# Performance work log

Hardware: AMD Instinct MI355X
Metric: run time of the kernel (lower is better)

## Reference

```python
import jax, jax.numpy as jnp
import numpy as np

K = 3  # kernel size per spatial dim (stride=1, same padding)
MED_IDX = (K * K * K - 1) // 2  # torch.median returns the lower median; 27 taps -> index 13


def setup_inputs() -> dict:
    key = jax.random.key(0)
    x = jax.random.normal(key, (2, 1, 160, 160, 160), dtype=jnp.float32)
    return {"x": x}


def _median_pool3d(x):
    # same padding for k=3, stride=1: pad 1 (reflect) on each side of D, H, W
    xp = jnp.pad(x, ((0, 0), (0, 0), (1, 1), (1, 1), (1, 1)), mode="reflect")
    B, C, D, H, W = x.shape
    # gather the 27 shifted views (static slices; loop over fixed small kernel is fine)
    windows = [
        xp[:, :, i:i + D, j:j + H, l:l + W]
        for i in range(K) for j in range(K) for l in range(K)
    ]
    stack = jnp.stack(windows, axis=0)  # [27, B, C, D, H, W]
    # torch .median(dim=-1)[0] over 27 taps == sorted value at index 13
    return jnp.sort(stack, axis=0)[MED_IDX]


def reference(x):
    return _median_pool3d(x)
```

## Files before the change

kernel.cpp:

```cpp
#include <hip/hip_runtime.h>


typedef __fp16 hf2 __attribute__((ext_vector_type(2)));

#define DEV __device__ __forceinline__

DEV hf2 hmin2(hf2 a, hf2 b) { return __builtin_elementwise_min(a, b); }
DEV hf2 hmax2(hf2 a, hf2 b) { return __builtin_elementwise_max(a, b); }
DEV void ce(hf2& a, hf2& b) { hf2 lo = hmin2(a, b); hf2 hi = hmax2(a, b); a = lo; b = hi; }
DEV hf2 pk2(float a, float b) { return __builtin_amdgcn_cvt_pkrtz(a, b); }

DEV void sort3(hf2& a, hf2& b, hf2& c) { ce(a, b); ce(a, c); ce(b, c); }

DEV void merge21(hf2 a0, hf2 a1, hf2 b0, hf2 z[3]) {
    hf2 e0 = a0, e1 = b0; ce(e0, e1);
    z[0] = e0; z[1] = a1; z[2] = e1; ce(z[1], z[2]);
}
DEV void merge22(hf2 a0, hf2 a1, hf2 b0, hf2 b1, hf2 z[4]) {
    hf2 p0 = a0, p1 = b0; ce(p0, p1);
    hf2 q0 = a1, q1 = b1; ce(q0, q1);
    z[0] = p0; z[1] = q0; z[2] = p1; ce(z[1], z[2]); z[3] = q1;
}
DEV void merge31(hf2 a0, hf2 a1, hf2 a2, hf2 b0, hf2 z[4]) {
    hf2 e[3]; merge21(a0, a2, b0, e);
    z[0] = e[0]; z[1] = a1; z[2] = e[1]; ce(z[1], z[2]); z[3] = e[2];
}
DEV void merge32(hf2 a0, hf2 a1, hf2 a2, hf2 b0, hf2 b1, hf2 z[5]) {
    hf2 e[3]; merge21(a0, a2, b0, e);
    hf2 o0 = a1, o1 = b1; ce(o0, o1);
    z[0] = e[0];
    z[1] = o0; z[2] = e[1]; ce(z[1], z[2]);
    z[3] = o1; z[4] = e[2]; ce(z[3], z[4]);
}
DEV void merge33(const hf2 a[3], const hf2 b[3], hf2 z[6]) {
    hf2 e[4]; merge22(a[0], a[2], b[0], b[2], e);
    hf2 o0 = a[1], o1 = b[1]; ce(o0, o1);
    z[0] = e[0];
    z[1] = o0; z[2] = e[1]; ce(z[1], z[2]);
    z[3] = o1; z[4] = e[2]; ce(z[3], z[4]);
    z[5] = e[3];
}
DEV void merge63(const hf2 a[6], const hf2 b[3], hf2 z[9]) {
    hf2 e[5]; merge32(a[0], a[2], a[4], b[0], b[2], e);
    hf2 o[4]; merge31(a[1], a[3], a[5], b[1], o);
    z[0] = e[0];
    z[1] = o[0]; z[2] = e[1]; ce(z[1], z[2]);
    z[3] = o[1]; z[4] = e[2]; ce(z[3], z[4]);
    z[5] = o[2]; z[6] = e[3]; ce(z[5], z[6]);
    z[7] = o[3]; z[8] = e[4]; ce(z[7], z[8]);
}
DEV void merge44(const hf2 a[4], const hf2 b[4], hf2 z[8]) {
    hf2 e[4]; merge22(a[0], a[2], b[0], b[2], e);
    hf2 o[4]; merge22(a[1], a[3], b[1], b[3], o);
    z[0] = e[0];
    z[1] = o[0]; z[2] = e[1]; ce(z[1], z[2]);
    z[3] = o[1]; z[4] = e[2]; ce(z[3], z[4]);
    z[5] = o[2]; z[6] = e[3]; ce(z[5], z[6]);
    z[7] = o[3];
}
DEV void merge55(const hf2 a[5], const hf2 b[5], hf2 z[10]) {
    hf2 ae[3] = {a[0], a[2], a[4]}, be[3] = {b[0], b[2], b[4]};
    hf2 e[6]; merge33(ae, be, e);
    hf2 o[4]; merge22(a[1], a[3], b[1], b[3], o);
    z[0] = e[0];
    z[1] = o[0]; z[2] = e[1]; ce(z[1], z[2]);
    z[3] = o[1]; z[4] = e[2]; ce(z[3], z[4]);
    z[5] = o[2]; z[6] = e[3]; ce(z[5], z[6]);
    z[7] = o[3]; z[8] = e[4]; ce(z[7], z[8]);
    z[9] = e[5];
}
DEV void merge99(const hf2 a[9], const hf2 b[9], hf2 z[18]) {
    hf2 ae[5] = {a[0], a[2], a[4], a[6], a[8]};
    hf2 be[5] = {b[0], b[2], b[4], b[6], b[8]};
    hf2 e[10]; merge55(ae, be, e);
    hf2 ao[4] = {a[1], a[3], a[5], a[7]};
    hf2 bo[4] = {b[1], b[3], b[5], b[7]};
    hf2 o[8]; merge44(ao, bo, o);
    z[0] = e[0];
#pragma unroll
    for (int i = 0; i < 8; i++) {
        z[2 * i + 1] = o[i];
        z[2 * i + 2] = e[i + 1];
        ce(z[2 * i + 1], z[2 * i + 2]);
    }
    z[17] = e[9];
}

DEV void compute_m(const float* __restrict__ pb, const int ro[3], int c0, int x0, int c3,
                   hf2 M[9]) {
    hf2 r[3][3];
#pragma unroll
    for (int i = 0; i < 3; i++) {
        const float* p = pb + ro[i];
        float a = p[c0];
        float2 bc = *reinterpret_cast<const float2*>(p + x0);
        float d = p[c3];
        r[i][0] = pk2(a, bc.x);
        r[i][1] = pk2(bc.x, bc.y);
        r[i][2] = pk2(bc.y, d);
    }
    sort3(r[0][0], r[0][1], r[0][2]);
    sort3(r[1][0], r[1][1], r[1][2]);
    sort3(r[2][0], r[2][1], r[2][2]);
    hf2 s6[6]; merge33(r[0], r[1], s6);
    merge63(s6, r[2], M);
}

DEV hf2 sel13(const hf2 E[18], const hf2 R[9]) {
    hf2 m = E[13];
#pragma unroll
    for (int i = 0; i < 9; i++) m = hmin2(m, hmax2(R[i], E[12 - i]));
    return m;
}

constexpr int Bb = 2, Dd = 160, Hh = 160, Ww = 160;
constexpr int HW = Hh * Ww;
constexpr int WP = Ww / 2;
constexpr int TP = Hh * WP;
constexpr int CH = 10;
constexpr int NCH = Dd / CH;
constexpr int TOTAL = Bb * NCH * TP;

__global__ __launch_bounds__(256) void MedianPool3d_68994354642979_kernel(
    const float* __restrict__ in, float* __restrict__ out) {
    int tid = blockIdx.x * 256 + threadIdx.x;
    if (tid >= TOTAL) return;
    int t = tid % TP;
    int co = tid / TP;
    int b = co >> 4;
    int chunk = co & 15;
    int y = t / WP;
    int px = t - y * WP;
    int x0 = px * 2;

    int ym = (y == 0) ? 1 : y - 1;
    int yp = (y == Hh - 1) ? Hh - 2 : y + 1;
    int ro[3] = {ym * Ww, y * Ww, yp * Ww};
    int c0 = (x0 == 0) ? 1 : x0 - 1;
    int c3 = (x0 == Ww - 2) ? (Ww - 2) : x0 + 2;

    const float* base = in + (size_t)b * Dd * HW;
    float* ob = out + (size_t)b * Dd * HW;
    int z0 = chunk * CH;

    auto planeptr = [&](int p) {
        if (p < 0) p = -p;
        if (p >= Dd) p = 2 * Dd - 2 - p;
        return base + (size_t)p * HW;
    };

    hf2 SS[4][9];
    compute_m(planeptr(z0 - 1), ro, c0, x0, c3, SS[0]);
    compute_m(planeptr(z0),     ro, c0, x0, c3, SS[1]);
    compute_m(planeptr(z0 + 1), ro, c0, x0, c3, SS[2]);

#pragma unroll
    for (int j = 0; j < CH / 2; j++) {
        int z = z0 + 2 * j;
        int sm1 = (2 * j) & 3;
        int s0  = (2 * j + 1) & 3;
        int s1  = (2 * j + 2) & 3;
        int s2  = (2 * j + 3) & 3;

        compute_m(planeptr(z + 2), ro, c0, x0, c3, SS[s2]);

        hf2 E[18];
        merge99(SS[s0], SS[s1], E);
        hf2 med0 = sel13(E, SS[sm1]);
        hf2 med1 = sel13(E, SS[s2]);

        float* o0 = ob + (size_t)z * HW + ro[1] + x0;
        float* o1 = o0 + HW;
        *reinterpret_cast<float2*>(o0) = make_float2((float)med0[0], (float)med0[1]);
        *reinterpret_cast<float2*>(o1) = make_float2((float)med1[0], (float)med1[1]);

        if (j < CH / 2 - 1)
            compute_m(planeptr(z + 3), ro, c0, x0, c3, SS[sm1]);
    }
}

extern "C" void kernel_launch(void* const* d_in, const int* in_sizes, int n_in,
                              void* d_out, int out_size, void* d_ws, size_t ws_size,
                              hipStream_t stream) {
    const float* x = (const float*)d_in[0];
    float* out = (float*)d_out;
    constexpr int threads = 256;
    constexpr int blocks = TOTAL / threads;
    MedianPool3d_68994354642979_kernel<<<blocks, threads, 0, stream>>>(x, out);
}
```

Before: 31.51 us.

## Split plane load from sort and prefetch raw planes one iteration ahead

Plane loading is split out from the per-plane sorting network so raw float data for the next two depth planes can be loaded into double-buffered registers one loop iteration before use. The goal is to hide global-load latency behind the merge and select arithmetic. A five-slot sorted-plane ring replaces the four-slot one, and launch bounds now request 4 blocks per CU. The extra live registers for prefetched planes may raise pressure and cause spills under the tighter occupancy bound.

```diff
diff --git a/kernel.cpp b/kernel.cpp
--- a/kernel.cpp
+++ b/kernel.cpp
@@ -86,22 +86,28 @@
     z[17] = e[9];
 }
 
-DEV void compute_m(const float* __restrict__ pb, const int ro[3], int c0, int x0, int c3,
-                   hf2 M[9]) {
-    hf2 r[3][3];
+DEV void load_plane(const float* __restrict__ pb, const int ro[3], int c0, int x0, int c3,
+                    float R[12]) {
 #pragma unroll
     for (int i = 0; i < 3; i++) {
         const float* p = pb + ro[i];
-        float a = p[c0];
+        R[i * 4 + 0] = p[c0];
         float2 bc = *reinterpret_cast<const float2*>(p + x0);
-        float d = p[c3];
-        r[i][0] = pk2(a, bc.x);
-        r[i][1] = pk2(bc.x, bc.y);
-        r[i][2] = pk2(bc.y, d);
-    }
-    sort3(r[0][0], r[0][1], r[0][2]);
-    sort3(r[1][0], r[1][1], r[1][2]);
-    sort3(r[2][0], r[2][1], r[2][2]);
+        R[i * 4 + 1] = bc.x;
+        R[i * 4 + 2] = bc.y;
+        R[i * 4 + 3] = p[c3];
+    }
+}
+
+DEV void sort_plane(const float R[12], hf2 M[9]) {
+    hf2 r[3][3];
+#pragma unroll
+    for (int i = 0; i < 3; i++) {
+        r[i][0] = pk2(R[i * 4 + 0], R[i * 4 + 1]);
+        r[i][1] = pk2(R[i * 4 + 1], R[i * 4 + 2]);
+        r[i][2] = pk2(R[i * 4 + 2], R[i * 4 + 3]);
+        sort3(r[i][0], r[i][1], r[i][2]);
+    }
     hf2 s6[6]; merge33(r[0], r[1], s6);
     merge63(s6, r[2], M);
 }
@@ -121,7 +127,7 @@
 constexpr int NCH = Dd / CH;
 constexpr int TOTAL = Bb * NCH * TP;
 
-__global__ __launch_bounds__(256) void MedianPool3d_68994354642979_kernel(
+__global__ __launch_bounds__(256, 4) void MedianPool3d_68994354642979_kernel(
     const float* __restrict__ in, float* __restrict__ out) {
     int tid = blockIdx.x * 256 + threadIdx.x;
     if (tid >= TOTAL) return;
@@ -149,33 +155,49 @@
         return base + (size_t)p * HW;
     };
 
-    hf2 SS[4][9];
-    compute_m(planeptr(z0 - 1), ro, c0, x0, c3, SS[0]);
-    compute_m(planeptr(z0),     ro, c0, x0, c3, SS[1]);
-    compute_m(planeptr(z0 + 1), ro, c0, x0, c3, SS[2]);
+    hf2 SS[5][9];
+    float RT[2][2][12];
+
+    {
+        float P0[12], P1[12], P2[12];
+        load_plane(planeptr(z0 - 1), ro, c0, x0, c3, P0);
+        load_plane(planeptr(z0),     ro, c0, x0, c3, P1);
+        load_plane(planeptr(z0 + 1), ro, c0, x0, c3, P2);
+        sort_plane(P0, SS[0]);
+        sort_plane(P1, SS[1]);
+        sort_plane(P2, SS[2]);
+    }
+    load_plane(planeptr(z0 + 2), ro, c0, x0, c3, RT[0][0]);
+    load_plane(planeptr(z0 + 3), ro, c0, x0, c3, RT[0][1]);
 
 #pragma unroll
     for (int j = 0; j < CH / 2; j++) {
-        int z = z0 + 2 * j;
-        int sm1 = (2 * j) & 3;
-        int s0  = (2 * j + 1) & 3;
-        int s1  = (2 * j + 2) & 3;
-        int s2  = (2 * j + 3) & 3;
-
-        compute_m(planeptr(z + 2), ro, c0, x0, c3, SS[s2]);
+        const int z = z0 + 2 * j;
+        const int sA = (2 * j) % 5;
+        const int sB = (2 * j + 1) % 5;
+        const int sC = (2 * j + 2) % 5;
+        const int sD = (2 * j + 3) % 5;
+        const int sE = (2 * j + 4) % 5;
+        const int cb = j & 1, nb = cb ^ 1;
+
+        if (j + 1 < CH / 2) {
+            load_plane(planeptr(z + 4), ro, c0, x0, c3, RT[nb][0]);
+            if (2 * (j + 1) + 3 <= CH)
+                load_plane(planeptr(z + 5), ro, c0, x0, c3, RT[nb][1]);
+        }
+
+        sort_plane(RT[cb][0], SS[sD]);
+        if (2 * j + 3 <= CH) sort_plane(RT[cb][1], SS[sE]);
 
         hf2 E[18];
-        merge99(SS[s0], SS[s1], E);
-        hf2 med0 = sel13(E, SS[sm1]);
-        hf2 med1 = sel13(E, SS[s2]);
+        merge99(SS[sB], SS[sC], E);
+        hf2 med0 = sel13(E, SS[sA]);
+        hf2 med1 = sel13(E, SS[sD]);
 
         float* o0 = ob + (size_t)z * HW + ro[1] + x0;
         float* o1 = o0 + HW;
         *reinterpret_cast<float2*>(o0) = make_float2((float)med0[0], (float)med0[1]);
         *reinterpret_cast<float2*>(o1) = make_float2((float)med1[0], (float)med1[1]);
-
-        if (j < CH / 2 - 1)
-            compute_m(planeptr(z + 3), ro, c0, x0, c3, SS[sm1]);
     }
 }
 
```

Measured after the change: 31.58 us. About the same (+0.2%).

## Process four columns per thread with hf4 sorting networks and float4 I/O

Applied to the files above, without the earlier changes.

Each thread now covers four x positions instead of two. Taps are packed into 4-wide half vectors, so each min/max operates on two packed pairs, and loads and stores use float4. The depth chunk shrinks from 10 to 8, the launch-bounds occupancy hint is raised to 4, and the thread index is decomposed differently. Doubling the work per thread doubles register state and halves the thread count, which risks spills or lower occupancy.

```diff
diff --git a/kernel.cpp b/kernel.cpp
--- a/kernel.cpp
+++ b/kernel.cpp
@@ -2,66 +2,68 @@
 
 
 typedef __fp16 hf2 __attribute__((ext_vector_type(2)));
+typedef __fp16 hf4 __attribute__((ext_vector_type(4)));
 
 #define DEV __device__ __forceinline__
 
-DEV hf2 hmin2(hf2 a, hf2 b) { return __builtin_elementwise_min(a, b); }
-DEV hf2 hmax2(hf2 a, hf2 b) { return __builtin_elementwise_max(a, b); }
-DEV void ce(hf2& a, hf2& b) { hf2 lo = hmin2(a, b); hf2 hi = hmax2(a, b); a = lo; b = hi; }
+DEV hf4 hmin4(hf4 a, hf4 b) { return __builtin_elementwise_min(a, b); }
+DEV hf4 hmax4(hf4 a, hf4 b) { return __builtin_elementwise_max(a, b); }
+DEV void ce(hf4& a, hf4& b) { hf4 lo = hmin4(a, b); hf4 hi = hmax4(a, b); a = lo; b = hi; }
 DEV hf2 pk2(float a, float b) { return __builtin_amdgcn_cvt_pkrtz(a, b); }
+DEV hf4 cat(hf2 a, hf2 b) { return __builtin_shufflevector(a, b, 0, 1, 2, 3); }
 
-DEV void sort3(hf2& a, hf2& b, hf2& c) { ce(a, b); ce(a, c); ce(b, c); }
+DEV void sort3(hf4& a, hf4& b, hf4& c) { ce(a, b); ce(a, c); ce(b, c); }
 
-DEV void merge21(hf2 a0, hf2 a1, hf2 b0, hf2 z[3]) {
-    hf2 e0 = a0, e1 = b0; ce(e0, e1);
+DEV void merge21(hf4 a0, hf4 a1, hf4 b0, hf4 z[3]) {
+    hf4 e0 = a0, e1 = b0; ce(e0, e1);
     z[0] = e0; z[1] = a1; z[2] = e1; ce(z[1], z[2]);
 }
-DEV void merge22(hf2 a0, hf2 a1, hf2 b0, hf2 b1, hf2 z[4]) {
-    hf2 p0 = a0, p1 = b0; ce(p0, p1);
-    hf2 q0 = a1, q1 = b1; ce(q0, q1);
+DEV void merge22(hf4 a0, hf4 a1, hf4 b0, hf4 b1, hf4 z[4]) {
+    hf4 p0 = a0, p1 = b0; ce(p0, p1);
+    hf4 q0 = a1, q1 = b1; ce(q0, q1);
     z[0] = p0; z[1] = q0; z[2] = p1; ce(z[1], z[2]); z[3] = q1;
 }
-DEV void merge31(hf2 a0, hf2 a1, hf2 a2, hf2 b0, hf2 z[4]) {
-    hf2 e[3]; merge21(a0, a2, b0, e);
+DEV void merge31(hf4 a0, hf4 a1, hf4 a2, hf4 b0, hf4 z[4]) {
+    hf4 e[3]; merge21(a0, a2, b0, e);
     z[0] = e[0]; z[1] = a1; z[2] = e[1]; ce(z[1], z[2]); z[3] = e[2];
 }
-DEV void merge32(hf2 a0, hf2 a1, hf2 a2, hf2 b0, hf2 b1, hf2 z[5]) {
-    hf2 e[3]; merge21(a0, a2, b0, e);
-    hf2 o0 = a1, o1 = b1; ce(o0, o1);
+DEV void merge32(hf4 a0, hf4 a1, hf4 a2, hf4 b0, hf4 b1, hf4 z[5]) {
+    hf4 e[3]; merge21(a0, a2, b0, e);
+    hf4 o0 = a1, o1 = b1; ce(o0, o1);
     z[0] = e[0];
     z[1] = o0; z[2] = e[1]; ce(z[1], z[2]);
     z[3] = o1; z[4] = e[2]; ce(z[3], z[4]);
 }
-DEV void merge33(const hf2 a[3], const hf2 b[3], hf2 z[6]) {
-    hf2 e[4]; merge22(a[0], a[2], b[0], b[2], e);
-    hf2 o0 = a[1], o1 = b[1]; ce(o0, o1);
+DEV void merge33(const hf4 a[3], const hf4 b[3], hf4 z[6]) {
+    hf4 e[4]; merge22(a[0], a[2], b[0], b[2], e);
+    hf4 o0 = a[1], o1 = b[1]; ce(o0, o1);
     z[0] = e[0];
     z[1] = o0; z[2] = e[1]; ce(z[1], z[2]);
     z[3] = o1; z[4] = e[2]; ce(z[3], z[4]);
     z[5] = e[3];
 }
-DEV void merge63(const hf2 a[6], const hf2 b[3], hf2 z[9]) {
-    hf2 e[5]; merge32(a[0], a[2], a[4], b[0], b[2], e);
-    hf2 o[4]; merge31(a[1], a[3], a[5], b[1], o);
+DEV void merge63(const hf4 a[6], const hf4 b[3], hf4 z[9]) {
+    hf4 e[5]; merge32(a[0], a[2], a[4], b[0], b[2], e);
+    hf4 o[4]; merge31(a[1], a[3], a[5], b[1], o);
     z[0] = e[0];
     z[1] = o[0]; z[2] = e[1]; ce(z[1], z[2]);
     z[3] = o[1]; z[4] = e[2]; ce(z[3], z[4]);
     z[5] = o[2]; z[6] = e[3]; ce(z[5], z[6]);
     z[7] = o[3]; z[8] = e[4]; ce(z[7], z[8]);
 }
-DEV void merge44(const hf2 a[4], const hf2 b[4], hf2 z[8]) {
-    hf2 e[4]; merge22(a[0], a[2], b[0], b[2], e);
-    hf2 o[4]; merge22(a[1], a[3], b[1], b[3], o);
+DEV void merge44(const hf4 a[4], const hf4 b[4], hf4 z[8]) {
+    hf4 e[4]; merge22(a[0], a[2], b[0], b[2], e);
+    hf4 o[4]; merge22(a[1], a[3], b[1], b[3], o);
     z[0] = e[0];
     z[1] = o[0]; z[2] = e[1]; ce(z[1], z[2]);
     z[3] = o[1]; z[4] = e[2]; ce(z[3], z[4]);
     z[5] = o[2]; z[6] = e[3]; ce(z[5], z[6]);
     z[7] = o[3];
 }
-DEV void merge55(const hf2 a[5], const hf2 b[5], hf2 z[10]) {
-    hf2 ae[3] = {a[0], a[2], a[4]}, be[3] = {b[0], b[2], b[4]};
-    hf2 e[6]; merge33(ae, be, e);
-    hf2 o[4]; merge22(a[1], a[3], b[1], b[3], o);
+DEV void merge55(const hf4 a[5], const hf4 b[5], hf4 z[10]) {
+    hf4 ae[3] = {a[0], a[2], a[4]}, be[3] = {b[0], b[2], b[4]};
+    hf4 e[6]; merge33(ae, be, e);
+    hf4 o[4]; merge22(a[1], a[3], b[1], b[3], o);
     z[0] = e[0];
     z[1] = o[0]; z[2] = e[1]; ce(z[1], z[2]);
     z[3] = o[1]; z[4] = e[2]; ce(z[3], z[4]);
@@ -69,13 +71,13 @@
     z[7] = o[3]; z[8] = e[4]; ce(z[7], z[8]);
     z[9] = e[5];
 }
-DEV void merge99(const hf2 a[9], const hf2 b[9], hf2 z[18]) {
-    hf2 ae[5] = {a[0], a[2], a[4], a[6], a[8]};
-    hf2 be[5] = {b[0], b[2], b[4], b[6], b[8]};
-    hf2 e[10]; merge55(ae, be, e);
-    hf2 ao[4] = {a[1], a[3], a[5], a[7]};
-    hf2 bo[4] = {b[1], b[3], b[5], b[7]};
-    hf2 o[8]; merge44(ao, bo, o);
+DEV void merge99(const hf4 a[9], const hf4 b[9], hf4 z[18]) {
+    hf4 ae[5] = {a[0], a[2], a[4], a[6], a[8]};
+    hf4 be[5] = {b[0], b[2], b[4], b[6], b[8]};
+    hf4 e[10]; merge55(ae, be, e);
+    hf4 ao[4] = {a[1], a[3], a[5], a[7]};
+    hf4 bo[4] = {b[1], b[3], b[5], b[7]};
+    hf4 o[8]; merge44(ao, bo, o);
     z[0] = e[0];
 #pragma unroll
     for (int i = 0; i < 8; i++) {
@@ -86,58 +88,60 @@
     z[17] = e[9];
 }
 
-DEV void compute_m(const float* __restrict__ pb, const int ro[3], int c0, int x0, int c3,
-                   hf2 M[9]) {
-    hf2 r[3][3];
+DEV void sort_plane(const float* __restrict__ pb, const int ro[3], int cL, int x0, int cR,
+                    hf4 M[9]) {
+    hf4 r[3][3];
 #pragma unroll
     for (int i = 0; i < 3; i++) {
         const float* p = pb + ro[i];
-        float a = p[c0];
-        float2 bc = *reinterpret_cast<const float2*>(p + x0);
-        float d = p[c3];
-        r[i][0] = pk2(a, bc.x);
-        r[i][1] = pk2(bc.x, bc.y);
-        r[i][2] = pk2(bc.y, d);
+        float a = p[cL];
+        float4 v = *reinterpret_cast<const float4*>(p + x0);
+        float d = p[cR];
+        hf2 pAL = pk2(a, v.x);
+        hf2 pAC = pk2(v.x, v.y);
+        hf2 pSH = pk2(v.y, v.z);
+        hf2 pBC = pk2(v.z, v.w);
+        hf2 pBR = pk2(v.w, d);
+        r[i][0] = cat(pAL, pSH);
+        r[i][1] = cat(pAC, pBC);
+        r[i][2] = cat(pSH, pBR);
+        sort3(r[i][0], r[i][1], r[i][2]);
     }
-    sort3(r[0][0], r[0][1], r[0][2]);
-    sort3(r[1][0], r[1][1], r[1][2]);
-    sort3(r[2][0], r[2][1], r[2][2]);
-    hf2 s6[6]; merge33(r[0], r[1], s6);
+    hf4 s6[6]; merge33(r[0], r[1], s6);
     merge63(s6, r[2], M);
 }
 
-DEV hf2 sel13(const hf2 E[18], const hf2 R[9]) {
-    hf2 m = E[13];
+DEV hf4 sel13(const hf4 E[18], const hf4 R[9]) {
+    hf4 m = E[13];
 #pragma unroll
-    for (int i = 0; i < 9; i++) m = hmin2(m, hmax2(R[i], E[12 - i]));
+    for (int i = 0; i < 9; i++) m = hmin4(m, hmax4(R[i], E[12 - i]));
     return m;
 }
 
 constexpr int Bb = 2, Dd = 160, Hh = 160, Ww = 160;
 constexpr int HW = Hh * Ww;
-constexpr int WP = Ww / 2;
-constexpr int TP = Hh * WP;
-constexpr int CH = 10;
+constexpr int WQ = Ww / 4;
+constexpr int TPC = Hh * WQ;
+constexpr int CH = 8;
 constexpr int NCH = Dd / CH;
-constexpr int TOTAL = Bb * NCH * TP;
+constexpr int TOTAL = Bb * NCH * TPC;
 
-__global__ __launch_bounds__(256) void MedianPool3d_68994354642979_kernel(
+__global__ __launch_bounds__(256, 4) void MedianPool3d_68994354642979_kernel(
     const float* __restrict__ in, float* __restrict__ out) {
     int tid = blockIdx.x * 256 + threadIdx.x;
-    if (tid >= TOTAL) return;
-    int t = tid % TP;
-    int co = tid / TP;
-    int b = co >> 4;
-    int chunk = co & 15;
-    int y = t / WP;
-    int px = t - y * WP;
-    int x0 = px * 2;
+    int q = tid % WQ;
+    int rest = tid / WQ;
+    int y = rest % Hh;
+    rest /= Hh;
+    int chunk = rest % NCH;
+    int b = rest / NCH;
+    int x0 = q * 4;
 
     int ym = (y == 0) ? 1 : y - 1;
     int yp = (y == Hh - 1) ? Hh - 2 : y + 1;
     int ro[3] = {ym * Ww, y * Ww, yp * Ww};
-    int c0 = (x0 == 0) ? 1 : x0 - 1;
-    int c3 = (x0 == Ww - 2) ? (Ww - 2) : x0 + 2;
+    int cL = (x0 == 0) ? 1 : x0 - 1;
+    int cR = (x0 + 4 == Ww) ? (Ww - 2) : x0 + 4;
 
     const float* base = in + (size_t)b * Dd * HW;
     float* ob = out + (size_t)b * Dd * HW;
@@ -149,33 +153,35 @@
         return base + (size_t)p * HW;
     };
 
-    hf2 SS[4][9];
-    compute_m(planeptr(z0 - 1), ro, c0, x0, c3, SS[0]);
-    compute_m(planeptr(z0),     ro, c0, x0, c3, SS[1]);
-    compute_m(planeptr(z0 + 1), ro, c0, x0, c3, SS[2]);
+    hf4 SS[4][9];
+    sort_plane(planeptr(z0 - 1), ro, cL, x0, cR, SS[0]);
+    sort_plane(planeptr(z0),     ro, cL, x0, cR, SS[1]);
+    sort_plane(planeptr(z0 + 1), ro, cL, x0, cR, SS[2]);
 
 #pragma unroll
     for (int j = 0; j < CH / 2; j++) {
-        int z = z0 + 2 * j;
-        int sm1 = (2 * j) & 3;
-        int s0  = (2 * j + 1) & 3;
-        int s1  = (2 * j + 2) & 3;
-        int s2  = (2 * j + 3) & 3;
+        const int z = z0 + 2 * j;
+        const int sA = (2 * j) & 3;
+        const int sB = (2 * j + 1) & 3;
+        const int sC = (2 * j + 2) & 3;
+        const int sD = (2 * j + 3) & 3;
 
-        compute_m(planeptr(z + 2), ro, c0, x0, c3, SS[s2]);
+        sort_plane(planeptr(z + 2), ro, cL, x0, cR, SS[sD]);
 
-        hf2 E[18];
-        merge99(SS[s0], SS[s1], E);
-        hf2 med0 = sel13(E, SS[sm1]);
-        hf2 med1 = sel13(E, SS[s2]);
+        hf4 E[18];
+        merge99(SS[sB], SS[sC], E);
+        hf4 m0 = sel13(E, SS[sA]);
+        hf4 m1 = sel13(E, SS[sD]);
 
         float* o0 = ob + (size_t)z * HW + ro[1] + x0;
         float* o1 = o0 + HW;
-        *reinterpret_cast<float2*>(o0) = make_float2((float)med0[0], (float)med0[1]);
-        *reinterpret_cast<float2*>(o1) = make_float2((float)med1[0], (float)med1[1]);
+        *reinterpret_cast<float4*>(o0) =
+            make_float4((float)m0.x, (float)m0.y, (float)m0.z, (float)m0.w);
+        *reinterpret_cast<float4*>(o1) =
+            make_float4((float)m1.x, (float)m1.y, (float)m1.z, (float)m1.w);
 
         if (j < CH / 2 - 1)
-            compute_m(planeptr(z + 3), ro, c0, x0, c3, SS[sm1]);
+            sort_plane(planeptr(z + 3), ro, cL, x0, cR, SS[sA]);
     }
 }
 
```

New measurement: 28.35 us. 10.0% less time.
